# Performance work log

Measured on AMD Instinct MI355X. Metric: run time of the kernel, lower is better.

## Reference

```python
import jax, jax.numpy as jnp
import numpy as np

B, E, H, T = 32768, 64, 128, 12  # batch, embedding_dim, decoder_h_dim, pred_len


def setup_inputs() -> dict:
    key = jax.random.key(0)
    ks = jax.random.split(key, 13)
    f = lambda k, shape: jax.random.normal(k, shape, dtype=jnp.float32) * 0.05
    return {
        "last_pos": f(ks[0], (B, 2)),
        "last_pos_rel": f(ks[1], (B, 2)),
        "h0": f(ks[2], (1, B, H)),
        "c0": f(ks[3], (1, B, H)),
        "pred_ped_speed": jax.random.uniform(ks[4], (T, B, 1), dtype=jnp.float32),
        # spatial_embedding: Linear(3, E)
        "W_se": f(ks[5], (E, 3)),
        "b_se": f(ks[6], (E,)),
        # single-layer LSTM(E -> H), torch gate order [i, f, g, o]
        "W_ih": f(ks[7], (4 * H, E)),
        "W_hh": f(ks[8], (4 * H, H)),
        "b_ih": f(ks[9], (4 * H,)),
        "b_hh": f(ks[10], (4 * H,)),
        # hidden2pos: Linear(H, 2)
        "W_hp": f(ks[11], (2, H)),
        "b_hp": f(ks[12], (2,)),
    }


def reference(last_pos, last_pos_rel, h0, c0, pred_ped_speed,
              W_se, b_se, W_ih, W_hh, b_ih, b_hh, W_hp, b_hp):
    # train_or_test == 0 path: speed comes straight from pred_ped_speed
    Tlen = pred_ped_speed.shape[0]
    b_lstm = b_ih + b_hh
    # initial decoder input: embed concat([last_pos_rel, speed_0])  -> [B, E]
    x0 = jnp.concatenate([last_pos_rel, pred_ped_speed[0]], axis=1) @ W_se.T + b_se

    def step(carry, t):
        h, c, x, lp = carry  # h,c: [B,H]; x: [B,E]; lp: [B,2]
        gates = x @ W_ih.T + h @ W_hh.T + b_lstm           # [B, 4H]
        i, f_, g, o = jnp.split(gates, 4, axis=1)
        c = jax.nn.sigmoid(f_) * c + jax.nn.sigmoid(i) * jnp.tanh(g)
        h = jax.nn.sigmoid(o) * jnp.tanh(c)
        rel = h @ W_hp.T + b_hp                            # [B, 2]
        lp = rel + lp                                      # curr_pos -> last_pos
        # speed for next step; at final step torch keeps the previous speed
        spd = pred_ped_speed[jnp.minimum(t + 1, Tlen - 1)]
        x = jnp.concatenate([rel, spd], axis=1) @ W_se.T + b_se
        return (h, c, x, lp), rel

    (h, c, _, _), rels = jax.lax.scan(
        step, (h0[0], c0[0], x0, last_pos), jnp.arange(Tlen))
    # pred_traj_fake_rel: [T, B, 2]; final hidden state: [1, B, H]
    return rels, h[None]
```

## Files before the change

### kernel.cpp

```cpp
#include <hip/hip_runtime.h>

#define T_LEN 12
#define B_N   32768
#define H_N   128
#define BM    64

typedef __attribute__((ext_vector_type(8))) __bf16 bf16x8;
typedef __attribute__((ext_vector_type(8))) short  short8v;
typedef __attribute__((ext_vector_type(4))) float  f32x4;

__device__ __forceinline__ unsigned short f2bf(float f) {
  unsigned int u = __builtin_bit_cast(unsigned int, f);
  u += 0x7fffu + ((u >> 16) & 1u);
  return (unsigned short)(u >> 16);
}
__device__ __forceinline__ float sigm_p(float x) {
  return __builtin_amdgcn_rcpf(1.f + __builtin_amdgcn_exp2f(x));
}
__device__ __forceinline__ float tanh_p(float x) {
  return __builtin_fmaf(-2.f, __builtin_amdgcn_rcpf(__builtin_amdgcn_exp2f(x) + 1.f), 1.f);
}
__device__ __forceinline__ float tanh_c(float x) {
  return tanh_p(2.8853900817779268f * x);
}

__global__ void prep_kernel(const float* __restrict__ Wih, const float* __restrict__ Whh,
                            const float* __restrict__ bih, const float* __restrict__ bhh,
                            const float* __restrict__ Wse, const float* __restrict__ bse,
                            const float* __restrict__ Whp, const float* __restrict__ bhp,
                            unsigned short* __restrict__ WfA, unsigned short* __restrict__ pBg,
                            float* __restrict__ u, float* __restrict__ w0,
                            float* __restrict__ G) {
  const float SCL[4] = {-1.4426950408889634f, -1.4426950408889634f,
                         2.8853900817779268f, -1.4426950408889634f};
  int i = blockIdx.x * 256 + threadIdx.x;
  if (i < 65536) {
    int row = i >> 7, k = i & 127;
    float s = Whh[row * 128 + k];
    float wh0 = Whp[k], wh1 = Whp[128 + k];
    for (int e = 0; e < 64; ++e)
      s += Wih[row * 64 + e] * (Wse[e * 3 + 0] * wh0 + Wse[e * 3 + 1] * wh1);
    int g = row >> 7, unit = row & 127, w = unit >> 4, l15 = unit & 15;
    int ks = k >> 5, kg = (k >> 3) & 3, j = k & 7, l = kg * 16 + l15;
    WfA[((g * 4 + ks) * 512 + w * 64 + l) * 8 + j] = f2bf(s * SCL[g]);
  } else if (i < 65536 + 2048) {
    int j = i - 65536;
    int n = j >> 2, which = j & 3, g = n >> 7;
    float s = 0.f;
    if (which < 2) {
      for (int e = 0; e < 64; ++e) s += Wih[n * 64 + e] * Wse[e * 3 + which];
      G[n * 2 + which] = s * SCL[g];
    } else if (which == 2) {
      for (int e = 0; e < 64; ++e) s += Wih[n * 64 + e] * Wse[e * 3 + 2];
      u[n] = s * SCL[g];
    } else {
      for (int e = 0; e < 64; ++e)
        s += Wih[n * 64 + e] * (bse[e] + Wse[e * 3 + 0] * bhp[0] + Wse[e * 3 + 1] * bhp[1]);
      w0[n] = (bih[n] + bhh[n] + s) * SCL[g];
    }
  } else if (i < 65536 + 2048 + 2048) {
    int idx = i - 65536 - 2048;
    int ks = idx >> 9, l = (idx >> 3) & 63, j = idx & 7;
    int c = l & 15, kg = l >> 4;
    pBg[idx] = (c < 2) ? f2bf(Whp[c * 128 + ks * 32 + kg * 8 + j]) : (unsigned short)0;
  }
}

__launch_bounds__(1024, 4)
__global__ void decoder_kernel(const float* __restrict__ lpr,
                               const float* __restrict__ h0,
                               const float* __restrict__ c0,
                               const float* __restrict__ pps,
                               const float* __restrict__ Whp,
                               const float* __restrict__ bhp,
                               const unsigned short* __restrict__ WfA,
                               const unsigned short* __restrict__ pBg,
                               const float* __restrict__ u,
                               const float* __restrict__ w0,
                               const float* __restrict__ G,
                               float* __restrict__ out_rel,
                               float* __restrict__ out_h) {
  __shared__ unsigned short WfL[65536];
  __shared__ unsigned short hA[BM * 128];
  __shared__ unsigned short pBL[2048];
  __shared__ float spdL[T_LEN * BM];
  __shared__ float dbuf[BM * 2];
  __shared__ float GL[1024];

  const int tid  = threadIdx.x;
  const int wav  = tid >> 6;
  const int wc   = wav & 7;
  const int wr   = wav >> 3;
  const int l    = tid & 63;
  const int l15  = l & 15;
  const int lg   = l >> 4;
  const int brow = blockIdx.x * BM;
  const int nh   = wc * 16 + l15;
  const int rowb = wr * 32;
  const int swzA = (l15 & 7) << 4;
  char* hB = (char*)hA;

#pragma unroll
  for (int it = 0; it < 8; ++it) {
    int idx = it * 1024 + tid;
    *(short8v*)(WfL + idx * 8) = *(const short8v*)(WfA + idx * 8);
  }
  if (tid < 256) *(short8v*)(pBL + tid * 8) = *(const short8v*)(pBg + tid * 8);
  GL[tid & 1023] = G[tid & 1023];
  if (tid < T_LEN * BM) spdL[tid] = pps[(tid >> 6) * B_N + brow + (tid & 63)];

  float w0r[4], ur[4];
#pragma unroll
  for (int g = 0; g < 4; ++g) { w0r[g] = w0[g * 128 + nh]; ur[g] = u[g * 128 + nh]; }

  f32x4 cst[2];
#pragma unroll
  for (int rt = 0; rt < 2; ++rt)
#pragma unroll
    for (int r = 0; r < 4; ++r)
      cst[rt][r] = c0[(brow + rowb + rt * 16 + lg * 4 + r) * H_N + nh];

  {
    int row = tid >> 4, k0 = (tid & 15) * 8;
    const float* src = h0 + (brow + row) * H_N + k0;
    unsigned short tmp[8];
#pragma unroll
    for (int j = 0; j < 8; ++j) tmp[j] = f2bf(src[j]);
    *(short8v*)(hB + ((row * 256 + k0 * 2) ^ ((row & 7) << 4))) = *(short8v*)tmp;
  }
  {
    int dot = tid >> 3, part = tid & 7;
    int row = dot >> 1, jj = dot & 1;
    float s = 0.f;
    const float* hrow = h0 + (brow + row) * H_N + part * 16;
    const float* wrow = Whp + jj * 128 + part * 16;
#pragma unroll
    for (int k = 0; k < 16; ++k) s += hrow[k] * wrow[k];
    s += __shfl_xor(s, 1); s += __shfl_xor(s, 2); s += __shfl_xor(s, 4);
    if (part == 0) dbuf[dot] = lpr[(brow + row) * 2 + jj] - bhp[jj] - s;
  }
  const float bhpr = (l15 < 2) ? bhp[l15] : 0.f;

#pragma unroll 1
  for (int t = 0; t < T_LEN; ++t) {
    __syncthreads();

    f32x4 acc[4][2];
#pragma unroll
    for (int g = 0; g < 4; ++g)
#pragma unroll
      for (int rt = 0; rt < 2; ++rt)
        acc[g][rt] = (f32x4){w0r[g], w0r[g], w0r[g], w0r[g]};
    f32x4 relC = (f32x4){0.f, 0.f, 0.f, 0.f};

#pragma unroll
    for (int ks = 0; ks < 4; ++ks) {
      bf16x8 a0 = __builtin_bit_cast(bf16x8,
          *(short8v*)(hB + (((rowb + l15) * 256 + ks * 64 + lg * 16) ^ swzA)));
      bf16x8 a1 = __builtin_bit_cast(bf16x8,
          *(short8v*)(hB + (((rowb + 16 + l15) * 256 + ks * 64 + lg * 16) ^ swzA)));
      bf16x8 b0 = __builtin_bit_cast(bf16x8, *(short8v*)(WfL + ((0 * 4 + ks) * 512 + wc * 64 + l) * 8));
      bf16x8 b1 = __builtin_bit_cast(bf16x8, *(short8v*)(WfL + ((1 * 4 + ks) * 512 + wc * 64 + l) * 8));
      bf16x8 b2 = __builtin_bit_cast(bf16x8, *(short8v*)(WfL + ((2 * 4 + ks) * 512 + wc * 64 + l) * 8));
      bf16x8 b3 = __builtin_bit_cast(bf16x8, *(short8v*)(WfL + ((3 * 4 + ks) * 512 + wc * 64 + l) * 8));
      acc[0][0] = __builtin_amdgcn_mfma_f32_16x16x32_bf16(a0, b0, acc[0][0], 0, 0, 0);
      acc[0][1] = __builtin_amdgcn_mfma_f32_16x16x32_bf16(a1, b0, acc[0][1], 0, 0, 0);
      acc[1][0] = __builtin_amdgcn_mfma_f32_16x16x32_bf16(a0, b1, acc[1][0], 0, 0, 0);
      acc[1][1] = __builtin_amdgcn_mfma_f32_16x16x32_bf16(a1, b1, acc[1][1], 0, 0, 0);
      acc[2][0] = __builtin_amdgcn_mfma_f32_16x16x32_bf16(a0, b2, acc[2][0], 0, 0, 0);
      acc[2][1] = __builtin_amdgcn_mfma_f32_16x16x32_bf16(a1, b2, acc[2][1], 0, 0, 0);
      acc[3][0] = __builtin_amdgcn_mfma_f32_16x16x32_bf16(a0, b3, acc[3][0], 0, 0, 0);
      acc[3][1] = __builtin_amdgcn_mfma_f32_16x16x32_bf16(a1, b3, acc[3][1], 0, 0, 0);
      if (wc < 2 && t > 0) {
        bf16x8 pb = __builtin_bit_cast(bf16x8, *(short8v*)(pBL + (ks * 64 + l) * 8));
        relC = __builtin_amdgcn_mfma_f32_16x16x32_bf16(wc == 0 ? a0 : a1, pb, relC, 0, 0, 0);
      }
    }
    if (wc < 2 && t > 0 && l15 < 2) {
#pragma unroll
      for (int r = 0; r < 4; ++r)
        out_rel[(size_t)(t - 1) * B_N * 2 + (brow + rowb + wc * 16 + lg * 4 + r) * 2 + l15] = relC[r] + bhpr;
    }

    __syncthreads();

#pragma unroll
    for (int rt = 0; rt < 2; ++rt) {
      const f32x4 spdv = *(const f32x4*)(spdL + t * BM + rowb + rt * 16 + lg * 4);
      if (t == 0) {
#pragma unroll
        for (int r = 0; r < 4; ++r) {
          int row = rowb + rt * 16 + lg * 4 + r;
          float d0 = dbuf[row * 2 + 0], d1 = dbuf[row * 2 + 1];
#pragma unroll
          for (int g = 0; g < 4; ++g)
            acc[g][rt][r] += d0 * GL[(g * 128 + nh) * 2 + 0] + d1 * GL[(g * 128 + nh) * 2 + 1];
        }
      }
#pragma unroll
      for (int r = 0; r < 4; ++r) {
        int row = rowb + rt * 16 + lg * 4 + r;
        float spd = spdv[r];
        float gi = __builtin_fmaf(spd, ur[0], acc[0][rt][r]);
        float gf = __builtin_fmaf(spd, ur[1], acc[1][rt][r]);
        float gg = __builtin_fmaf(spd, ur[2], acc[2][rt][r]);
        float go = __builtin_fmaf(spd, ur[3], acc[3][rt][r]);
        float cn = sigm_p(gf) * cst[rt][r] + sigm_p(gi) * tanh_p(gg);
        cst[rt][r] = cn;
        float h = sigm_p(go) * tanh_c(cn);
        *(unsigned short*)(hB + ((row * 256 + nh * 2) ^ ((row & 7) << 4))) = f2bf(h);
        if (t == T_LEN - 1) out_h[(brow + row) * H_N + nh] = h;
      }
    }
  }

  __syncthreads();
  if (wc < 2) {
    f32x4 relC = (f32x4){0.f, 0.f, 0.f, 0.f};
#pragma unroll
    for (int ks = 0; ks < 4; ++ks) {
      bf16x8 a = __builtin_bit_cast(bf16x8,
          *(short8v*)(hB + (((rowb + wc * 16 + l15) * 256 + ks * 64 + lg * 16) ^ swzA)));
      bf16x8 pb = __builtin_bit_cast(bf16x8, *(short8v*)(pBL + (ks * 64 + l) * 8));
      relC = __builtin_amdgcn_mfma_f32_16x16x32_bf16(a, pb, relC, 0, 0, 0);
    }
    if (l15 < 2) {
#pragma unroll
      for (int r = 0; r < 4; ++r)
        out_rel[(size_t)(T_LEN - 1) * B_N * 2 + (brow + rowb + wc * 16 + lg * 4 + r) * 2 + l15] = relC[r] + bhpr;
    }
  }
}

extern "C" void kernel_launch(void* const* d_in, const int* in_sizes, int n_in,
                              void* d_out, int out_size, void* d_ws, size_t ws_size,
                              hipStream_t stream) {
  const float* lpr  = (const float*)d_in[1];
  const float* h0   = (const float*)d_in[2];
  const float* c0   = (const float*)d_in[3];
  const float* pps  = (const float*)d_in[4];
  const float* W_se = (const float*)d_in[5];
  const float* b_se = (const float*)d_in[6];
  const float* W_ih = (const float*)d_in[7];
  const float* W_hh = (const float*)d_in[8];
  const float* b_ih = (const float*)d_in[9];
  const float* b_hh = (const float*)d_in[10];
  const float* W_hp = (const float*)d_in[11];
  const float* b_hp = (const float*)d_in[12];

  unsigned short* WfA = (unsigned short*)d_ws;
  unsigned short* pBg = (unsigned short*)((char*)d_ws + 131072);
  float* u  = (float*)((char*)d_ws + 135168);
  float* w0 = (float*)((char*)d_ws + 137216);
  float* G  = (float*)((char*)d_ws + 139264);

  float* out_rel = (float*)d_out;
  float* out_h   = out_rel + (size_t)T_LEN * B_N * 2;

  hipLaunchKernelGGL(prep_kernel, dim3((65536 + 4096 + 255) / 256), dim3(256), 0, stream,
                     W_ih, W_hh, b_ih, b_hh, W_se, b_se, W_hp, b_hp,
                     WfA, pBg, u, w0, G);
  hipLaunchKernelGGL(decoder_kernel, dim3(B_N / BM), dim3(1024), 0, stream,
                     lpr, h0, c0, pps, W_hp, b_hp, WfA, pBg, u, w0, G,
                     out_rel, out_h);
}
```

Baseline: 217.2 us.

## Halve the batch tile, stream LSTM weights from global, double-buffer hidden state

Drops the 128KB LDS copy of the fused LSTM weights and reads each B fragment directly from global memory inside the recurrence. The batch tile shrinks to 32 rows with 512-thread blocks, so more blocks can reside on each CU. The hidden state is now ping-ponged between two LDS buffers, which removes one __syncthreads per step, and the k-slice order is rotated by t to vary access patterns. The cost is that every block re-fetches the full weight matrix every timestep through the cache hierarchy, which sharply raises L1/L2 traffic.

```diff
diff --git a/kernel.cpp b/kernel.cpp
--- a/kernel.cpp
+++ b/kernel.cpp
@@ -3,7 +3,7 @@
 #define T_LEN 12
 #define B_N   32768
 #define H_N   128
-#define BM    64
+#define BM    32
 
 typedef __attribute__((ext_vector_type(8))) __bf16 bf16x8;
 typedef __attribute__((ext_vector_type(8))) short  short8v;
@@ -66,7 +66,7 @@
   }
 }
 
-__launch_bounds__(1024, 4)
+__launch_bounds__(512, 4)
 __global__ void decoder_kernel(const float* __restrict__ lpr,
                                const float* __restrict__ h0,
                                const float* __restrict__ c0,
@@ -80,8 +80,7 @@
                                const float* __restrict__ G,
                                float* __restrict__ out_rel,
                                float* __restrict__ out_h) {
-  __shared__ unsigned short WfL[65536];
-  __shared__ unsigned short hA[BM * 128];
+  __shared__ unsigned short hA[2][BM * 128];
   __shared__ unsigned short pBL[2048];
   __shared__ float spdL[T_LEN * BM];
   __shared__ float dbuf[BM * 2];
@@ -89,25 +88,16 @@
 
   const int tid  = threadIdx.x;
   const int wav  = tid >> 6;
-  const int wc   = wav & 7;
-  const int wr   = wav >> 3;
   const int l    = tid & 63;
   const int l15  = l & 15;
   const int lg   = l >> 4;
   const int brow = blockIdx.x * BM;
-  const int nh   = wc * 16 + l15;
-  const int rowb = wr * 32;
+  const int nh   = wav * 16 + l15;
   const int swzA = (l15 & 7) << 4;
-  char* hB = (char*)hA;
-
-#pragma unroll
-  for (int it = 0; it < 8; ++it) {
-    int idx = it * 1024 + tid;
-    *(short8v*)(WfL + idx * 8) = *(const short8v*)(WfA + idx * 8);
-  }
+
   if (tid < 256) *(short8v*)(pBL + tid * 8) = *(const short8v*)(pBg + tid * 8);
-  GL[tid & 1023] = G[tid & 1023];
-  if (tid < T_LEN * BM) spdL[tid] = pps[(tid >> 6) * B_N + brow + (tid & 63)];
+  for (int i = tid; i < 1024; i += 512) GL[i] = G[i];
+  if (tid < T_LEN * BM) spdL[tid] = pps[(tid >> 5) * B_N + brow + (tid & 31)];
 
   float w0r[4], ur[4];
 #pragma unroll
@@ -118,7 +108,7 @@
   for (int rt = 0; rt < 2; ++rt)
 #pragma unroll
     for (int r = 0; r < 4; ++r)
-      cst[rt][r] = c0[(brow + rowb + rt * 16 + lg * 4 + r) * H_N + nh];
+      cst[rt][r] = c0[(brow + rt * 16 + lg * 4 + r) * H_N + nh];
 
   {
     int row = tid >> 4, k0 = (tid & 15) * 8;
@@ -126,7 +116,7 @@
     unsigned short tmp[8];
 #pragma unroll
     for (int j = 0; j < 8; ++j) tmp[j] = f2bf(src[j]);
-    *(short8v*)(hB + ((row * 256 + k0 * 2) ^ ((row & 7) << 4))) = *(short8v*)tmp;
+    *(short8v*)((char*)&hA[0][0] + ((row * 256 + k0 * 2) ^ ((row & 7) << 4))) = *(short8v*)tmp;
   }
   {
     int dot = tid >> 3, part = tid & 7;
@@ -141,6 +131,9 @@
   }
   const float bhpr = (l15 < 2) ? bhp[l15] : 0.f;
 
+  char* rb = (char*)&hA[0][0];
+  char* wbuf = (char*)&hA[1][0];
+
 #pragma unroll 1
   for (int t = 0; t < T_LEN; ++t) {
     __syncthreads();
@@ -155,14 +148,15 @@
 
 #pragma unroll
     for (int ks = 0; ks < 4; ++ks) {
+      const int kk = (ks + t) & 3;
       bf16x8 a0 = __builtin_bit_cast(bf16x8,
-          *(short8v*)(hB + (((rowb + l15) * 256 + ks * 64 + lg * 16) ^ swzA)));
+          *(short8v*)(rb + ((l15 * 256 + kk * 64 + lg * 16) ^ swzA)));
       bf16x8 a1 = __builtin_bit_cast(bf16x8,
-          *(short8v*)(hB + (((rowb + 16 + l15) * 256 + ks * 64 + lg * 16) ^ swzA)));
-      bf16x8 b0 = __builtin_bit_cast(bf16x8, *(short8v*)(WfL + ((0 * 4 + ks) * 512 + wc * 64 + l) * 8));
-      bf16x8 b1 = __builtin_bit_cast(bf16x8, *(short8v*)(WfL + ((1 * 4 + ks) * 512 + wc * 64 + l) * 8));
-      bf16x8 b2 = __builtin_bit_cast(bf16x8, *(short8v*)(WfL + ((2 * 4 + ks) * 512 + wc * 64 + l) * 8));
-      bf16x8 b3 = __builtin_bit_cast(bf16x8, *(short8v*)(WfL + ((3 * 4 + ks) * 512 + wc * 64 + l) * 8));
+          *(short8v*)(rb + (((16 + l15) * 256 + kk * 64 + lg * 16) ^ swzA)));
+      bf16x8 b0 = __builtin_bit_cast(bf16x8, *(const short8v*)(WfA + ((0 * 4 + kk) * 512 + wav * 64 + l) * 8));
+      bf16x8 b1 = __builtin_bit_cast(bf16x8, *(const short8v*)(WfA + ((1 * 4 + kk) * 512 + wav * 64 + l) * 8));
+      bf16x8 b2 = __builtin_bit_cast(bf16x8, *(const short8v*)(WfA + ((2 * 4 + kk) * 512 + wav * 64 + l) * 8));
+      bf16x8 b3 = __builtin_bit_cast(bf16x8, *(const short8v*)(WfA + ((3 * 4 + kk) * 512 + wav * 64 + l) * 8));
       acc[0][0] = __builtin_amdgcn_mfma_f32_16x16x32_bf16(a0, b0, acc[0][0], 0, 0, 0);
       acc[0][1] = __builtin_amdgcn_mfma_f32_16x16x32_bf16(a1, b0, acc[0][1], 0, 0, 0);
       acc[1][0] = __builtin_amdgcn_mfma_f32_16x16x32_bf16(a0, b1, acc[1][0], 0, 0, 0);
@@ -171,26 +165,24 @@
       acc[2][1] = __builtin_amdgcn_mfma_f32_16x16x32_bf16(a1, b2, acc[2][1], 0, 0, 0);
       acc[3][0] = __builtin_amdgcn_mfma_f32_16x16x32_bf16(a0, b3, acc[3][0], 0, 0, 0);
       acc[3][1] = __builtin_amdgcn_mfma_f32_16x16x32_bf16(a1, b3, acc[3][1], 0, 0, 0);
-      if (wc < 2 && t > 0) {
-        bf16x8 pb = __builtin_bit_cast(bf16x8, *(short8v*)(pBL + (ks * 64 + l) * 8));
-        relC = __builtin_amdgcn_mfma_f32_16x16x32_bf16(wc == 0 ? a0 : a1, pb, relC, 0, 0, 0);
+      if (wav < 2 && t > 0) {
+        bf16x8 pb = __builtin_bit_cast(bf16x8, *(short8v*)(pBL + (kk * 64 + l) * 8));
+        relC = __builtin_amdgcn_mfma_f32_16x16x32_bf16(wav == 0 ? a0 : a1, pb, relC, 0, 0, 0);
       }
     }
-    if (wc < 2 && t > 0 && l15 < 2) {
+    if (wav < 2 && t > 0 && l15 < 2) {
 #pragma unroll
       for (int r = 0; r < 4; ++r)
-        out_rel[(size_t)(t - 1) * B_N * 2 + (brow + rowb + wc * 16 + lg * 4 + r) * 2 + l15] = relC[r] + bhpr;
-    }
-
-    __syncthreads();
+        out_rel[(size_t)(t - 1) * B_N * 2 + (brow + wav * 16 + lg * 4 + r) * 2 + l15] = relC[r] + bhpr;
+    }
 
 #pragma unroll
     for (int rt = 0; rt < 2; ++rt) {
-      const f32x4 spdv = *(const f32x4*)(spdL + t * BM + rowb + rt * 16 + lg * 4);
+      const f32x4 spdv = *(const f32x4*)(spdL + t * BM + rt * 16 + lg * 4);
       if (t == 0) {
 #pragma unroll
         for (int r = 0; r < 4; ++r) {
-          int row = rowb + rt * 16 + lg * 4 + r;
+          int row = rt * 16 + lg * 4 + r;
           float d0 = dbuf[row * 2 + 0], d1 = dbuf[row * 2 + 1];
 #pragma unroll
           for (int g = 0; g < 4; ++g)
@@ -199,7 +191,7 @@
       }
 #pragma unroll
       for (int r = 0; r < 4; ++r) {
-        int row = rowb + rt * 16 + lg * 4 + r;
+        int row = rt * 16 + lg * 4 + r;
         float spd = spdv[r];
         float gi = __builtin_fmaf(spd, ur[0], acc[0][rt][r]);
         float gf = __builtin_fmaf(spd, ur[1], acc[1][rt][r]);
@@ -208,26 +200,27 @@
         float cn = sigm_p(gf) * cst[rt][r] + sigm_p(gi) * tanh_p(gg);
         cst[rt][r] = cn;
         float h = sigm_p(go) * tanh_c(cn);
-        *(unsigned short*)(hB + ((row * 256 + nh * 2) ^ ((row & 7) << 4))) = f2bf(h);
+        *(unsigned short*)(wbuf + ((row * 256 + nh * 2) ^ ((row & 7) << 4))) = f2bf(h);
         if (t == T_LEN - 1) out_h[(brow + row) * H_N + nh] = h;
       }
     }
+    char* tmpp = rb; rb = wbuf; wbuf = tmpp;
   }
 
   __syncthreads();
-  if (wc < 2) {
+  if (wav < 2) {
     f32x4 relC = (f32x4){0.f, 0.f, 0.f, 0.f};
 #pragma unroll
     for (int ks = 0; ks < 4; ++ks) {
       bf16x8 a = __builtin_bit_cast(bf16x8,
-          *(short8v*)(hB + (((rowb + wc * 16 + l15) * 256 + ks * 64 + lg * 16) ^ swzA)));
+          *(short8v*)(rb + (((wav * 16 + l15) * 256 + ks * 64 + lg * 16) ^ swzA)));
       bf16x8 pb = __builtin_bit_cast(bf16x8, *(short8v*)(pBL + (ks * 64 + l) * 8));
       relC = __builtin_amdgcn_mfma_f32_16x16x32_bf16(a, pb, relC, 0, 0, 0);
     }
     if (l15 < 2) {
 #pragma unroll
       for (int r = 0; r < 4; ++r)
-        out_rel[(size_t)(T_LEN - 1) * B_N * 2 + (brow + rowb + wc * 16 + lg * 4 + r) * 2 + l15] = relC[r] + bhpr;
+        out_rel[(size_t)(T_LEN - 1) * B_N * 2 + (brow + wav * 16 + lg * 4 + r) * 2 + l15] = relC[r] + bhpr;
     }
   }
 }
@@ -260,7 +253,7 @@
   hipLaunchKernelGGL(prep_kernel, dim3((65536 + 4096 + 255) / 256), dim3(256), 0, stream,
                      W_ih, W_hh, b_ih, b_hh, W_se, b_se, W_hp, b_hp,
                      WfA, pBg, u, w0, G);
-  hipLaunchKernelGGL(decoder_kernel, dim3(B_N / BM), dim3(1024), 0, stream,
+  hipLaunchKernelGGL(decoder_kernel, dim3(B_N / BM), dim3(512), 0, stream,
                      lpr, h0, c0, pps, W_hp, b_hp, WfA, pBg, u, w0, G,
                      out_rel, out_h);
 }
```

After: 217.3 us. No clear change (+0.1%).
